# Optimization experiments

Measured on AMD Instinct MI355X. Metric: run time of the kernel, lower is better.

The kernel has to match this reference:

```python
import jax, jax.numpy as jnp
import numpy as np

D_MODEL, D_STATE, D_CONV, EXPAND = 1024, 16, 4, 2
D_INNER = EXPAND * D_MODEL
BATCH, SEQ = 2, 2048


def setup_inputs() -> dict:
    key = jax.random.key(0)
    ks = jax.random.split(key, 10)
    inv = lambda n: 1.0 / np.sqrt(n)
    return {
        "x": jax.random.normal(ks[0], (BATCH, SEQ, D_MODEL), jnp.float32),
        "in_proj_w": jax.random.uniform(ks[1], (2 * D_INNER, D_MODEL), jnp.float32, -inv(D_MODEL), inv(D_MODEL)),
        "conv_w": jax.random.uniform(ks[2], (D_INNER, D_INNER, D_CONV), jnp.float32, -inv(D_INNER * D_CONV), inv(D_INNER * D_CONV)),
        "conv_b": jax.random.uniform(ks[3], (D_INNER,), jnp.float32, -inv(D_INNER * D_CONV), inv(D_INNER * D_CONV)),
        "dt_w": jax.random.uniform(ks[4], (D_INNER, D_INNER), jnp.float32, -inv(D_INNER), inv(D_INNER)),
        "dt_b": jax.random.uniform(ks[5], (D_INNER,), jnp.float32, -inv(D_INNER), inv(D_INNER)),
        "A_log": jax.random.normal(ks[6], (D_INNER, D_STATE), jnp.float32) * 0.01,
        "D": jnp.ones((D_INNER,), jnp.float32),
        "B_w": jax.random.uniform(ks[7], (D_STATE, D_INNER), jnp.float32, -inv(D_INNER), inv(D_INNER)),
        "C_w": jax.random.uniform(ks[8], (D_STATE, D_INNER), jnp.float32, -inv(D_INNER), inv(D_INNER)),
        "out_w": jax.random.uniform(ks[9], (D_MODEL, D_INNER), jnp.float32, -inv(D_INNER), inv(D_INNER)),
    }


def _forward(x, in_proj_w, conv_w, conv_b, dt_w, dt_b, A_log, D, B_w, C_w, out_w):
    xz = x @ in_proj_w.T                      # [b, l, 2*d_inner]
    xc, z = jnp.split(xz, 2, axis=-1)
    # causal depthful conv1d (full channel mixing, left-padded)
    h = jnp.transpose(xc, (0, 2, 1))          # [b, d, l]
    h = jnp.pad(h, ((0, 0), (0, 0), (D_CONV - 1, 0)))
    h = jax.lax.conv_general_dilated(h, conv_w, (1,), 'VALID',
                                     dimension_numbers=('NCH', 'OIH', 'NCH'))
    h = h + conv_b[None, :, None]
    u = jnp.transpose(h, (0, 2, 1))           # [b, l, d_inner]

    dt = jnp.clip(jax.nn.sigmoid(u @ dt_w.T + dt_b), 1e-4, 1.0)  # [b, l, d]
    A = -jnp.exp(A_log)                       # [d, n]
    Bm = u @ B_w.T                            # [b, l, n]
    Cm = u @ C_w.T                            # [b, l, n]

    # time-major scan over the recurrence
    u_t = jnp.transpose(u, (1, 0, 2))
    dt_t = jnp.transpose(dt, (1, 0, 2))
    B_t = jnp.transpose(Bm, (1, 0, 2))
    C_t = jnp.transpose(Cm, (1, 0, 2))

    def step(state, inp):
        ut, dtt, bt, ct = inp                 # [b,d], [b,d], [b,n], [b,n]
        dA = jnp.exp(jnp.clip(dtt[:, :, None] * A, -5.0, 5.0))   # [b,d,n]
        dB = dtt[:, :, None] * bt[:, None, :] * ut[:, :, None]   # [b,d,n]
        state = dA * state + dB + 1e-6
        y = jnp.sum(state * ct[:, None, :], axis=-1) + D * ut    # [b,d]
        return state, y

    state0 = jnp.zeros((x.shape[0], D_INNER, D_STATE), x.dtype)
    _, ys = jax.lax.scan(step, state0, (u_t, dt_t, B_t, C_t))
    y = jnp.transpose(ys, (1, 0, 2))          # [b, l, d_inner]
    y = y * jax.nn.silu(z)
    return y @ out_w.T                        # [b, l, d_model]


def reference(x, in_proj_w, conv_w, conv_b, dt_w, dt_b, A_log, D, B_w, C_w, out_w):
    return _forward(x, in_proj_w, conv_w, conv_b, dt_w, dt_b, A_log, D, B_w, C_w, out_w)
```

## Files before the change

### kernel.cpp

```cpp
#include <hip/hip_runtime.h>

#define BATCHN 2
#define SEQL   2048
#define DM     1024
#define DI     2048
#define DSN    16
#define MTOT   (BATCHN * SEQL)
#define PADL   (SEQL + 3)
#define NC     64
#define CL     (SEQL / NC)
#define BCKS   8

typedef __attribute__((ext_vector_type(8))) __bf16 bf16x8;
typedef __attribute__((ext_vector_type(4))) float f32x4;

__device__ __forceinline__ unsigned short f2b(float f) {
    union { float f; unsigned u; } v; v.f = f;
    unsigned r = v.u + 0x7FFF + ((v.u >> 16) & 1);
    return (unsigned short)(r >> 16);
}
__device__ __forceinline__ float b2f(unsigned short b) {
    union { float f; unsigned u; } v; v.u = ((unsigned)b) << 16;
    return v.f;
}

__device__ __forceinline__ void gl_lds16(const void* g, void* l) {
    __builtin_amdgcn_global_load_lds(
        (const __attribute__((address_space(1))) unsigned int*)g,
        (__attribute__((address_space(3))) unsigned int*)l, 16, 0, 0);
}

__device__ __forceinline__ void swz(int& bx, int& by) {
    int gx = gridDim.x, gy = gridDim.y;
    int lin = blockIdx.y * gx + blockIdx.x;
    int xcd = lin & 7, k = lin >> 3;
    int rw = gx >> 1, rh = gy >> 2;
    by = (xcd >> 1) * rh + k / rw;
    bx = (xcd & 1) * rw + k % rw;
}

#define NB_CW4  (DI * DI / 4 / 256)
#define NB_TP   ((DM / 32) * (DI / 32))
#define NB_IPZ  (DI * DM / 4 / 256)
#define NB_DTW  (DI * DI / 4 / 256)
#define NB_OW   (DM * DI / 4 / 256)
#define NB_BW   (DSN * DI / 4 / 256 + 1)
#define NB_XCVT (MTOT * DM / 4 / 256)
#define NB_XZ   ((BATCHN * 3 * DM + 255) / 256)
#define NB_CVT_ALL (NB_CW4 + NB_TP + NB_IPZ + NB_DTW + NB_OW + 2 * NB_BW + NB_XCVT + NB_XZ)

__global__ void __launch_bounds__(256)
cvt_all(const float* __restrict__ x, const float* __restrict__ convw,
        const float* __restrict__ ipw, const float* __restrict__ dtw,
        const float* __restrict__ ow, const float* __restrict__ bw,
        const float* __restrict__ cw,
        unsigned short* __restrict__ xpad, unsigned short* __restrict__ wk,
        unsigned short* __restrict__ Pt, unsigned short* __restrict__ ipz,
        unsigned short* __restrict__ dtwb, unsigned short* __restrict__ owb,
        unsigned short* __restrict__ bcb)
{
    __shared__ float tile[32][33];
    int blk = blockIdx.x;
    int t = threadIdx.x;
    if (blk < NB_CW4) {
        int g = blk * 256 + t;
        int i = g * 4;
        const float4* cw4 = (const float4*)convw;
        float4 v0 = cw4[i + 0], v1 = cw4[i + 1], v2 = cw4[i + 2], v3 = cw4[i + 3];
#pragma unroll
        for (int k = 0; k < 4; ++k) {
            float e0 = (&v0.x)[k], e1 = (&v1.x)[k], e2 = (&v2.x)[k], e3 = (&v3.x)[k];
            ushort4 o;
            o.x = f2b(e0); o.y = f2b(e1); o.z = f2b(e2); o.w = f2b(e3);
            ((ushort4*)(wk + (size_t)k * DI * DI))[g] = o;
        }
        return;
    }
    blk -= NB_CW4;
    if (blk < NB_TP) {
        int ct = (blk & 31) * 32, it = (blk >> 5) * 32;
        int tx = t & 31, ty = t >> 5;
#pragma unroll
        for (int r = 0; r < 4; ++r)
            tile[ty + r * 8][tx] = ipw[(size_t)(it + ty + r * 8) * DM + ct + tx];
        __syncthreads();
#pragma unroll
        for (int r = 0; r < 4; ++r)
            Pt[(size_t)(ct + ty + r * 8) * DI + it + tx] = f2b(tile[tx][ty + r * 8]);
        return;
    }
    blk -= NB_TP;
    if (blk < NB_IPZ + NB_DTW + NB_OW + 2 * NB_BW) {
        const float* src;
        unsigned short* dst;
        int n4;
        if (blk < NB_IPZ) {
            src = ipw + (size_t)DI * DM; dst = ipz; n4 = DI * DM / 4;
        } else if ((blk -= NB_IPZ) < NB_DTW) {
            src = dtw; dst = dtwb; n4 = DI * DI / 4;
        } else if ((blk -= NB_DTW) < NB_OW) {
            src = ow; dst = owb; n4 = DM * DI / 4;
        } else if ((blk -= NB_OW) < NB_BW) {
            src = bw; dst = bcb; n4 = DSN * DI / 4;
        } else {
            blk -= NB_BW;
            src = cw; dst = bcb + (size_t)DSN * DI; n4 = DSN * DI / 4;
        }
        int i = blk * 256 + t;
        if (i < n4) {
            float4 v = ((const float4*)src)[i];
            ushort4 o;
            o.x = f2b(v.x); o.y = f2b(v.y); o.z = f2b(v.z); o.w = f2b(v.w);
            ((ushort4*)dst)[i] = o;
        }
        return;
    }
    blk -= NB_IPZ + NB_DTW + NB_OW + 2 * NB_BW;
    if (blk < NB_XCVT) {
        int i = blk * 256 + t;
        int b = i >> 19;
        float4 v = ((const float4*)x)[i];
        ushort4 o;
        o.x = f2b(v.x); o.y = f2b(v.y); o.z = f2b(v.z); o.w = f2b(v.w);
        ((ushort4*)xpad)[i + (b + 1) * (3 * DM / 4)] = o;
        return;
    }
    blk -= NB_XCVT;
    {
        int i = blk * 256 + t;
        if (i < BATCHN * 3 * DM) {
            int b = i / (3 * DM);
            int r = i % (3 * DM);
            xpad[(size_t)b * PADL * DM + r] = 0;
        }
    }
}

template<int MODE>
__global__ void __launch_bounds__(256)
gemm_bt(const unsigned short* __restrict__ Abase,
        const unsigned short* __restrict__ Bbase,
        const float* __restrict__ bias,
        unsigned short* __restrict__ out_bf,
        float* __restrict__ out_f,
        int K)
{
    __shared__ __align__(16) unsigned short As[128 * 64];
    __shared__ __align__(16) unsigned short Bs[128 * 64];

    const int t = threadIdx.x;
    const int lane = t & 63;
    const int wave = t >> 6;
    const int wm = wave & 1, wn = wave >> 1;
    int bx, by;
    swz(bx, by);
    const int m0 = by * 128, n0 = bx * 128;
    const int srow = t >> 3;
    const int scol = (t & 7) * 8;
    const int gcol = (((t & 7) ^ (srow & 7))) * 8;

    f32x4 acc[4][4];
#pragma unroll
    for (int i = 0; i < 4; ++i)
#pragma unroll
        for (int j = 0; j < 4; ++j)
            acc[i][j] = f32x4{0.f, 0.f, 0.f, 0.f};

    const unsigned short* arow[4];
    const unsigned short* brow[4];
#pragma unroll
    for (int i = 0; i < 4; ++i) {
        int rg = m0 + srow + i * 32;
        arow[i] = Abase + (size_t)rg * K;
        int ng = n0 + srow + i * 32;
        brow[i] = Bbase + (size_t)ng * K;
    }
    for (int k0 = 0; k0 < K; k0 += 64) {
#pragma unroll
        for (int i = 0; i < 4; ++i)
            gl_lds16(arow[i] + k0 + gcol, &As[(size_t)(srow + i * 32) * 64 + scol]);
#pragma unroll
        for (int i = 0; i < 4; ++i)
            gl_lds16(brow[i] + k0 + gcol, &Bs[(size_t)(srow + i * 32) * 64 + scol]);
        __syncthreads();
        const int qa = (lane >> 4) * 8;
        const int am = lane & 15;
        const int sw = (am & 7) << 3;
#pragma unroll
        for (int kk = 0; kk < 64; kk += 32) {
            bf16x8 af[4], bfv[4];
#pragma unroll
            for (int i = 0; i < 4; ++i)
                af[i] = *(const bf16x8*)&As[(wm * 64 + i * 16 + am) * 64 + ((kk + qa) ^ sw)];
#pragma unroll
            for (int j = 0; j < 4; ++j)
                bfv[j] = *(const bf16x8*)&Bs[(wn * 64 + j * 16 + am) * 64 + ((kk + qa) ^ sw)];
#pragma unroll
            for (int i = 0; i < 4; ++i)
#pragma unroll
                for (int j = 0; j < 4; ++j)
                    acc[i][j] = __builtin_amdgcn_mfma_f32_16x16x32_bf16(
                        af[i], bfv[j], acc[i][j], 0, 0, 0);
        }
        __syncthreads();
    }

    const int erow0 = m0 + wm * 64;
    const int ecol0 = n0 + wn * 64 + (lane & 15);
    const int rq = (lane >> 4) * 4;
#pragma unroll
    for (int i = 0; i < 4; ++i) {
#pragma unroll
        for (int j = 0; j < 4; ++j) {
            int col = ecol0 + j * 16;
#pragma unroll
            for (int r = 0; r < 4; ++r) {
                int row = erow0 + i * 16 + rq + r;
                float v = acc[i][j][r];
                if (MODE == 3) {
                    out_f[(size_t)row * DM + col] = v;
                } else {
                    out_bf[(size_t)row * DI + col] = f2b(v);
                }
            }
        }
    }
}

#define STAGE(buf, kt) do { \
    const int kc_ = ((kt) & NTM) << 6; \
    gl_lds16(pA + 0 * 64 * SA + kc_, &lds[(buf) * 16384 + ldsA + 0 * 4096]); \
    gl_lds16(pA + 1 * 64 * SA + kc_, &lds[(buf) * 16384 + ldsA + 1 * 4096]); \
    gl_lds16(pA + 2 * 64 * SA + kc_, &lds[(buf) * 16384 + ldsA + 2 * 4096]); \
    gl_lds16(pA + 3 * 64 * SA + kc_, &lds[(buf) * 16384 + ldsA + 3 * 4096]); \
    gl_lds16(pB + 0 * 64 * SB + kc_, &lds[32768 + (buf) * 8192 + ldsB + 0 * 4096]); \
    gl_lds16(pB + 1 * 64 * SB + kc_, &lds[32768 + (buf) * 8192 + ldsB + 1 * 4096]); \
} while (0)

#define LOADF(AF, BF, buf) do { \
    const unsigned short* _ab = &lds[(buf) * 16384 + arow]; \
    const unsigned short* _bb = &lds[32768 + (buf) * 8192 + brow]; \
    _Pragma("unroll") \
    for (int _i = 0; _i < 4; ++_i) { \
        AF[_i][0] = *(const bf16x8*)&_ab[_i * 1024 + c0]; \
        AF[_i][1] = *(const bf16x8*)&_ab[_i * 1024 + c1]; \
    } \
    _Pragma("unroll") \
    for (int _j = 0; _j < 4; ++_j) { \
        BF[_j][0] = *(const bf16x8*)&_bb[_j * 1024 + c0]; \
        BF[_j][1] = *(const bf16x8*)&_bb[_j * 1024 + c1]; \
    } \
} while (0)

#define MME(AF, BF) do { \
    _Pragma("unroll") \
    for (int _i = 0; _i < 4; ++_i) \
    _Pragma("unroll") \
    for (int _j = 0; _j < 4; ++_j) { \
        acc[_i][_j] = __builtin_amdgcn_mfma_f32_16x16x32_bf16(AF[_i][0], BF[_j][0], acc[_i][_j], 0, 0, 0); \
        acc[_i][_j] = __builtin_amdgcn_mfma_f32_16x16x32_bf16(AF[_i][1], BF[_j][1], acc[_i][_j], 0, 0, 0); \
    } \
} while (0)

template<int MODE>
__global__ void __launch_bounds__(512, 1)
gemm8(const unsigned short* __restrict__ Abase,
      const unsigned short* __restrict__ Bbase,
      const float* __restrict__ bias,
      unsigned short* __restrict__ out_bf,
      float* __restrict__ out_f)
{
    constexpr int K   = (MODE == 0) ? 1024 : (MODE == 1) ? 4096 : 2048;
    constexpr int SA  = (MODE == 2 || MODE == 4) ? 2048 : 1024;
    constexpr int SB  = (MODE == 0) ? 1024 : (MODE == 1) ? 4096 : 2048;
    constexpr int NT  = K / 64;
    constexpr int NTM = NT - 1;
    constexpr int NI  = NT / 2;
    (void)out_f;

    __shared__ __align__(16) unsigned short lds[49152];

    const int t = threadIdx.x;
    const int lane = t & 63;
    const int wave = t >> 6;
    const int wm = wave >> 1;
    const int wn = wave & 1;
    int bx, by;
    swz(bx, by);
    const int m0 = by * 256, n0 = bx * 128;

    const unsigned short* Ap;
    if (MODE == 0)      Ap = Abase + ((size_t)(m0 >> 11) * PADL + 3 + (m0 & 2047)) * DM;
    else if (MODE == 1) Ap = Abase + ((size_t)(m0 >> 11) * PADL + (m0 & 2047)) * DM;
    else if (MODE == 4) Ap = Abase + (size_t)blockIdx.z * DI * DI + (size_t)m0 * SA;
    else                Ap = Abase + (size_t)m0 * SA;
    const unsigned short* Bp = Bbase + (size_t)n0 * SB;

    const int strow = t >> 3;
    const int gcs = ((t & 7) ^ (strow & 7)) * 8;
    const unsigned short* pA = Ap + (size_t)strow * SA + gcs;
    const unsigned short* pB = Bp + (size_t)strow * SB + gcs;
    const int ldsA = t * 8;
    const int ldsB = t * 8;

    const int am = lane & 15;
    const int qa = (lane >> 4) << 3;
    const int sw = (am & 7) << 3;
    const int c0 = qa ^ sw;
    const int c1 = (32 + qa) ^ sw;
    const int arow = (wm * 64 + am) * 64;
    const int brow = (wn * 64 + am) * 64;

    f32x4 acc[4][4];
#pragma unroll
    for (int i = 0; i < 4; ++i)
#pragma unroll
        for (int j = 0; j < 4; ++j)
            acc[i][j] = f32x4{0.f, 0.f, 0.f, 0.f};

    bf16x8 aX[4][2], bX[4][2], aY[4][2], bY[4][2];

    STAGE(0, 0);
    STAGE(1, 1);
    asm volatile("s_waitcnt vmcnt(6)" ::: "memory");
    __builtin_amdgcn_s_barrier();
    __builtin_amdgcn_sched_barrier(0);
    LOADF(aX, bX, 0);

#pragma unroll 1
    for (int it = 0; it < NI; ++it) {
        asm volatile("s_waitcnt lgkmcnt(0)" ::: "memory");
        __builtin_amdgcn_s_barrier();
        __builtin_amdgcn_sched_barrier(0);
        STAGE(0, 2 * it + 2);
        asm volatile("s_waitcnt vmcnt(6)" ::: "memory");
        __builtin_amdgcn_s_barrier();
        __builtin_amdgcn_sched_barrier(0);
        LOADF(aY, bY, 1);
        __builtin_amdgcn_s_setprio(1);
        MME(aX, bX);
        __builtin_amdgcn_s_setprio(0);
        asm volatile("s_waitcnt lgkmcnt(0)" ::: "memory");
        __builtin_amdgcn_s_barrier();
        __builtin_amdgcn_sched_barrier(0);
        STAGE(1, 2 * it + 3);
        asm volatile("s_waitcnt vmcnt(6)" ::: "memory");
        __builtin_amdgcn_s_barrier();
        __builtin_amdgcn_sched_barrier(0);
        LOADF(aX, bX, 0);
        __builtin_amdgcn_s_setprio(1);
        MME(aY, bY);
        __builtin_amdgcn_s_setprio(0);
    }

    asm volatile("s_waitcnt vmcnt(0) lgkmcnt(0)" ::: "memory");

    const int rq = (lane >> 4) << 2;
    const int er = m0 + wm * 64;
    const int ec = n0 + wn * 64 + am;
#pragma unroll
    for (int mi = 0; mi < 4; ++mi) {
#pragma unroll
        for (int nj = 0; nj < 4; ++nj) {
            int col = ec + nj * 16;
#pragma unroll
            for (int r = 0; r < 4; ++r) {
                int row = er + mi * 16 + rq + r;
                float v = acc[mi][nj][r];
                if (MODE == 0) {
                    out_bf[(size_t)row * DI + col] = f2b(v);
                } else if (MODE == 1) {
                    v += bias[col];
                    out_bf[(size_t)row * DI + col] = f2b(v);
                } else if (MODE == 2) {
                    v += bias[col];
                    float s = 1.f / (1.f + __expf(-v));
                    s = fminf(fmaxf(s, 1e-4f), 1.f);
                    out_bf[(size_t)row * DI + col] = f2b(s);
                } else {
                    out_bf[(size_t)row * 4096 + (size_t)blockIdx.z * 1024 + col] = f2b(v);
                }
            }
        }
    }
}

__global__ void __launch_bounds__(256)
bc_mfma(const unsigned short* __restrict__ u,
        const unsigned short* __restrict__ w,
        float* __restrict__ pc)
{
    const int t = threadIdx.x;
    const int lane = t & 63;
    const int wave = t >> 6;
    const int ks = blockIdx.x;
    const int m0 = blockIdx.y * 128 + wave * 32;
    const int am = lane & 15, quad = lane >> 4;

    f32x4 acc[2][2];
#pragma unroll
    for (int i = 0; i < 2; ++i)
#pragma unroll
        for (int j = 0; j < 2; ++j)
            acc[i][j] = f32x4{0.f, 0.f, 0.f, 0.f};

    const int kbase = ks * (DI / BCKS);
    const unsigned short* ur0 = u + (size_t)(m0 + am) * DI;
    const unsigned short* ur1 = u + (size_t)(m0 + 16 + am) * DI;
    const unsigned short* wr0 = w + (size_t)am * DI;
    const unsigned short* wr1 = w + (size_t)(16 + am) * DI;
#pragma unroll 2
    for (int kk = 0; kk < DI / BCKS; kk += 32) {
        int k = kbase + kk + quad * 8;
        bf16x8 a0 = *(const bf16x8*)(ur0 + k);
        bf16x8 a1 = *(const bf16x8*)(ur1 + k);
        bf16x8 b0 = *(const bf16x8*)(wr0 + k);
        bf16x8 b1 = *(const bf16x8*)(wr1 + k);
        acc[0][0] = __builtin_amdgcn_mfma_f32_16x16x32_bf16(a0, b0, acc[0][0], 0, 0, 0);
        acc[0][1] = __builtin_amdgcn_mfma_f32_16x16x32_bf16(a0, b1, acc[0][1], 0, 0, 0);
        acc[1][0] = __builtin_amdgcn_mfma_f32_16x16x32_bf16(a1, b0, acc[1][0], 0, 0, 0);
        acc[1][1] = __builtin_amdgcn_mfma_f32_16x16x32_bf16(a1, b1, acc[1][1], 0, 0, 0);
    }
    float* base = pc + (size_t)ks * MTOT * 32;
#pragma unroll
    for (int i = 0; i < 2; ++i)
#pragma unroll
        for (int j = 0; j < 2; ++j)
#pragma unroll
            for (int r = 0; r < 4; ++r) {
                int row = m0 + i * 16 + quad * 4 + r;
                int col = j * 16 + am;
                base[(size_t)row * 32 + col] = acc[i][j][r];
            }
}

__global__ void __launch_bounds__(256)
scan_p1(const unsigned short* __restrict__ dt_bf,
        const unsigned short* __restrict__ u_bf,
        const float* __restrict__ pc,
        const float* __restrict__ A_log,
        float* __restrict__ Pbuf,
        float* __restrict__ Sb,
        float* __restrict__ bcf)
{
    const int t = threadIdx.x;
    const int blk = blockIdx.x;
    const int c  = blk & (NC - 1);
    const int dh = (blk >> 6) & 7;
    const int b  = blk >> 9;
    const int d  = dh * 256 + t;

    const size_t rowbase = (size_t)b * SEQL + (size_t)c * CL;

    __shared__ float sm[CL][32];
    for (int idx = t; idx < CL * 32; idx += 256) {
        int r = idx >> 5, n = idx & 31;
        size_t base = (rowbase + r) * 32 + n;
        float s = pc[base];
#pragma unroll
        for (int ks = 1; ks < BCKS; ++ks)
            s += pc[(size_t)ks * (MTOT * 32) + base];
        sm[r][n] = s;
        if (dh == 0) bcf[base] = s;
    }

    float Adn[16];
    {
        const float4* ar = (const float4*)(A_log + (size_t)d * DSN);
#pragma unroll
        for (int q = 0; q < 4; ++q) {
            float4 v = ar[q];
            Adn[q * 4 + 0] = -__expf(v.x);
            Adn[q * 4 + 1] = -__expf(v.y);
            Adn[q * 4 + 2] = -__expf(v.z);
            Adn[q * 4 + 3] = -__expf(v.w);
        }
    }
    float s[16], P[16];
#pragma unroll
    for (int n = 0; n < 16; ++n) { s[n] = 0.f; P[n] = 1.f; }

    __syncthreads();

    for (int l0 = 0; l0 < CL; l0 += 4) {
        float dt4[4], u4[4];
#pragma unroll
        for (int j = 0; j < 4; ++j) {
            size_t rb = rowbase + l0 + j;
            dt4[j] = b2f(dt_bf[rb * DI + d]);
            u4[j] = b2f(u_bf[rb * DI + d]);
        }
#pragma unroll
        for (int j = 0; j < 4; ++j) {
            const float4* Br = (const float4*)(&sm[l0 + j][0]);
            float Bn[16];
#pragma unroll
            for (int q = 0; q < 4; ++q) {
                float4 v = Br[q];
                Bn[q * 4 + 0] = v.x; Bn[q * 4 + 1] = v.y;
                Bn[q * 4 + 2] = v.z; Bn[q * 4 + 3] = v.w;
            }
            float dt = dt4[j];
            float dBu = dt * u4[j];
#pragma unroll
            for (int n = 0; n < 16; ++n) {
                float x = dt * Adn[n];
                x = fminf(fmaxf(x, -5.f), 5.f);
                float dA = __expf(x);
                P[n] *= dA;
                s[n] = dA * s[n] + (dBu * Bn[n] + 1e-6f);
            }
        }
    }
    size_t ob = (((size_t)c * BATCHN + b) * DI + d) * DSN;
#pragma unroll
    for (int q = 0; q < 4; ++q) {
        ((float4*)(Pbuf + ob))[q] = make_float4(P[q*4], P[q*4+1], P[q*4+2], P[q*4+3]);
        ((float4*)(Sb + ob))[q] = make_float4(s[q*4], s[q*4+1], s[q*4+2], s[q*4+3]);
    }
}

__global__ void __launch_bounds__(256)
scan_p2(const float* __restrict__ Pbuf,
        float* __restrict__ Sb)
{
    const int i = blockIdx.x * 256 + threadIdx.x;
    const int stride = BATCHN * DI * DSN;
    float s = 0.f;
    for (int c0 = 0; c0 < NC; c0 += 8) {
        float Pv[8], Sv[8];
#pragma unroll
        for (int j = 0; j < 8; ++j) {
            size_t idx = (size_t)(c0 + j) * stride + i;
            Pv[j] = Pbuf[idx];
            Sv[j] = Sb[idx];
        }
#pragma unroll
        for (int j = 0; j < 8; ++j) {
            size_t idx = (size_t)(c0 + j) * stride + i;
            Sb[idx] = s;
            s = Pv[j] * s + Sv[j];
        }
    }
}

__global__ void __launch_bounds__(256)
scan_p3(const unsigned short* __restrict__ dt_bf,
        const unsigned short* __restrict__ u_bf,
        const float* __restrict__ bcf,
        const unsigned short* __restrict__ z_bf,
        const float* __restrict__ A_log,
        const float* __restrict__ Dvec,
        const float* __restrict__ Ib,
        unsigned short* __restrict__ y_bf)
{
    const int t = threadIdx.x;
    const int blk = blockIdx.x;
    const int c  = blk & (NC - 1);
    const int dh = (blk >> 6) & 7;
    const int b  = blk >> 9;
    const int d  = dh * 256 + t;

    float Adn[16];
    {
        const float4* ar = (const float4*)(A_log + (size_t)d * DSN);
#pragma unroll
        for (int q = 0; q < 4; ++q) {
            float4 v = ar[q];
            Adn[q * 4 + 0] = -__expf(v.x);
            Adn[q * 4 + 1] = -__expf(v.y);
            Adn[q * 4 + 2] = -__expf(v.z);
            Adn[q * 4 + 3] = -__expf(v.w);
        }
    }
    const float Dd = Dvec[d];
    float s[16];
    {
        size_t ib = (((size_t)c * BATCHN + b) * DI + d) * DSN;
#pragma unroll
        for (int q = 0; q < 4; ++q) {
            float4 v = ((const float4*)(Ib + ib))[q];
            s[q * 4 + 0] = v.x; s[q * 4 + 1] = v.y;
            s[q * 4 + 2] = v.z; s[q * 4 + 3] = v.w;
        }
    }

    const size_t rowbase = (size_t)b * SEQL + (size_t)c * CL;
    for (int l0 = 0; l0 < CL; l0 += 4) {
        float dt4[4], u4[4], z4[4];
#pragma unroll
        for (int j = 0; j < 4; ++j) {
            size_t rb = rowbase + l0 + j;
            dt4[j] = b2f(dt_bf[rb * DI + d]);
            u4[j] = b2f(u_bf[rb * DI + d]);
            z4[j] = b2f(z_bf[rb * DI + d]);
        }
#pragma unroll
        for (int j = 0; j < 4; ++j) {
            size_t rb = rowbase + l0 + j;
            const float4* Br = (const float4*)(bcf + rb * 32);
            float Bn[16], Cn[16];
#pragma unroll
            for (int q = 0; q < 4; ++q) {
                float4 v = Br[q];
                Bn[q * 4 + 0] = v.x; Bn[q * 4 + 1] = v.y;
                Bn[q * 4 + 2] = v.z; Bn[q * 4 + 3] = v.w;
                float4 w = Br[q + 4];
                Cn[q * 4 + 0] = w.x; Cn[q * 4 + 1] = w.y;
                Cn[q * 4 + 2] = w.z; Cn[q * 4 + 3] = w.w;
            }
            float dt = dt4[j];
            float dBu = dt * u4[j];
            float y = 0.f;
#pragma unroll
            for (int n = 0; n < 16; ++n) {
                float x = dt * Adn[n];
                x = fminf(fmaxf(x, -5.f), 5.f);
                float dA = __expf(x);
                s[n] = dA * s[n] + (dBu * Bn[n] + 1e-6f);
                y += s[n] * Cn[n];
            }
            y += Dd * u4[j];
            float zz = z4[j];
            y *= zz / (1.f + __expf(-zz));
            y_bf[rb * DI + d] = f2b(y);
        }
    }
}

extern "C" void kernel_launch(void* const* d_in, const int* in_sizes, int n_in,
                              void* d_out, int out_size, void* d_ws, size_t ws_size,
                              hipStream_t stream) {
    const float* x     = (const float*)d_in[0];
    const float* ipw   = (const float*)d_in[1];
    const float* convw = (const float*)d_in[2];
    const float* convb = (const float*)d_in[3];
    const float* dtw   = (const float*)d_in[4];
    const float* dtb   = (const float*)d_in[5];
    const float* alog  = (const float*)d_in[6];
    const float* dvec  = (const float*)d_in[7];
    const float* bw    = (const float*)d_in[8];
    const float* cwm   = (const float*)d_in[9];
    const float* ow    = (const float*)d_in[10];
    float* out = (float*)d_out;

    char* ws = (char*)d_ws;
    unsigned short* wk_bf  = (unsigned short*)(ws);
    unsigned short* dt_bf  = (unsigned short*)(ws);
    float*          Pbuf   = (float*)(ws + 16777216);
    unsigned short* y_bf   = (unsigned short*)(ws + 16777216);
    unsigned short* mk_bf  = (unsigned short*)(ws + 33554432);
    float*          Sb     = (float*)(ws + 33554432);
    unsigned short* xpad   = (unsigned short*)(ws + 50331648);
    float*          pc_f   = (float*)(ws + 50331648);
    unsigned short* z_bf   = (unsigned short*)(ws + 58732544);
    unsigned short* Pt_bf  = (unsigned short*)(ws + 58732544);
    unsigned short* ipz_bf = (unsigned short*)(ws + 75509760);
    unsigned short* dtw_bf = (unsigned short*)(ws + 79704064);
    unsigned short* ow_bf  = (unsigned short*)(ws + 88092672);
    unsigned short* bc_bf  = (unsigned short*)(ws + 92286976);
    float*          bc_f   = (float*)(ws + 92418048);
    unsigned short* u_bf   = (unsigned short*)(ws + 92942336);

    cvt_all<<<NB_CVT_ALL, 256, 0, stream>>>(x, convw, ipw, dtw, ow, bw, cwm,
                                            xpad, wk_bf, Pt_bf, ipz_bf, dtw_bf,
                                            ow_bf, bc_bf);

    gemm8<4><<<dim3(8, 8, 4), 512, 0, stream>>>(wk_bf, Pt_bf, nullptr, mk_bf, nullptr);
    gemm8<0><<<dim3(16, 16), 512, 0, stream>>>(xpad, ipz_bf, nullptr, z_bf, nullptr);
    gemm8<1><<<dim3(16, 16), 512, 0, stream>>>(xpad, mk_bf, convb, u_bf, nullptr);
    bc_mfma<<<dim3(BCKS, MTOT / 128), 256, 0, stream>>>(u_bf, bc_bf, pc_f);
    gemm8<2><<<dim3(16, 16), 512, 0, stream>>>(u_bf, dtw_bf, dtb, dt_bf, nullptr);
    scan_p1<<<BATCHN * 8 * NC, 256, 0, stream>>>(dt_bf, u_bf, pc_f, alog, Pbuf, Sb, bc_f);
    scan_p2<<<BATCHN * DI * DSN / 256, 256, 0, stream>>>(Pbuf, Sb);
    scan_p3<<<BATCHN * 8 * NC, 256, 0, stream>>>(dt_bf, u_bf, bc_f, z_bf, alog, dvec, Sb, y_bf);
    gemm_bt<3><<<dim3(8, 32), 256, 0, stream>>>(y_bf, ow_bf, nullptr, nullptr, out, DI);
}
```

Measured before the change: 454.1 us.

## Split GEMM K dimension across two wave groups with LDS reduction

Restructures the gemm8 main loop so the 8 waves form two groups that each process half of the K range. Each wave now holds a 128x64 accumulator tile (8x4 MFMA tiles) and loads 32-wide K slices into separate LDS buffers. At the end the two groups' partial sums are combined through LDS before the epilogue. This raises the number of MFMAs per LDS fragment load and simplifies the pipeline, at the cost of doubled accumulator registers, an extra reduction pass with syncs, and shallower per-step K slices.

```diff
diff --git a/kernel.cpp b/kernel.cpp
--- a/kernel.cpp
+++ b/kernel.cpp
@@ -227,39 +227,14 @@
     }
 }
 
-#define STAGE(buf, kt) do { \
-    const int kc_ = ((kt) & NTM) << 6; \
-    gl_lds16(pA + 0 * 64 * SA + kc_, &lds[(buf) * 16384 + ldsA + 0 * 4096]); \
-    gl_lds16(pA + 1 * 64 * SA + kc_, &lds[(buf) * 16384 + ldsA + 1 * 4096]); \
-    gl_lds16(pA + 2 * 64 * SA + kc_, &lds[(buf) * 16384 + ldsA + 2 * 4096]); \
-    gl_lds16(pA + 3 * 64 * SA + kc_, &lds[(buf) * 16384 + ldsA + 3 * 4096]); \
-    gl_lds16(pB + 0 * 64 * SB + kc_, &lds[32768 + (buf) * 8192 + ldsB + 0 * 4096]); \
-    gl_lds16(pB + 1 * 64 * SB + kc_, &lds[32768 + (buf) * 8192 + ldsB + 1 * 4096]); \
-} while (0)
-
-#define LOADF(AF, BF, buf) do { \
-    const unsigned short* _ab = &lds[(buf) * 16384 + arow]; \
-    const unsigned short* _bb = &lds[32768 + (buf) * 8192 + brow]; \
-    _Pragma("unroll") \
-    for (int _i = 0; _i < 4; ++_i) { \
-        AF[_i][0] = *(const bf16x8*)&_ab[_i * 1024 + c0]; \
-        AF[_i][1] = *(const bf16x8*)&_ab[_i * 1024 + c1]; \
-    } \
-    _Pragma("unroll") \
-    for (int _j = 0; _j < 4; ++_j) { \
-        BF[_j][0] = *(const bf16x8*)&_bb[_j * 1024 + c0]; \
-        BF[_j][1] = *(const bf16x8*)&_bb[_j * 1024 + c1]; \
-    } \
-} while (0)
-
-#define MME(AF, BF) do { \
-    _Pragma("unroll") \
-    for (int _i = 0; _i < 4; ++_i) \
-    _Pragma("unroll") \
-    for (int _j = 0; _j < 4; ++_j) { \
-        acc[_i][_j] = __builtin_amdgcn_mfma_f32_16x16x32_bf16(AF[_i][0], BF[_j][0], acc[_i][_j], 0, 0, 0); \
-        acc[_i][_j] = __builtin_amdgcn_mfma_f32_16x16x32_bf16(AF[_i][1], BF[_j][1], acc[_i][_j], 0, 0, 0); \
-    } \
+
+#define STG2(buf, kt) do { const int kc_ = ((kt) & NTM) * 32; \
+    gl_lds16(pA0[0] + kc_, &lds[(buf) * 8192 + l8]); \
+    gl_lds16(pA1[0] + kc_, &lds[(buf) * 8192 + 4096 + l8]); \
+    gl_lds16(pB2[0] + kc_, &lds[32768 + (buf) * 4096 + l8]); \
+    gl_lds16(pA0[1] + kc_, &lds[16384 + (buf) * 8192 + l8]); \
+    gl_lds16(pA1[1] + kc_, &lds[16384 + (buf) * 8192 + 4096 + l8]); \
+    gl_lds16(pB2[1] + kc_, &lds[40960 + (buf) * 4096 + l8]); \
 } while (0)
 
 template<int MODE>
@@ -273,9 +248,9 @@
     constexpr int K   = (MODE == 0) ? 1024 : (MODE == 1) ? 4096 : 2048;
     constexpr int SA  = (MODE == 2 || MODE == 4) ? 2048 : 1024;
     constexpr int SB  = (MODE == 0) ? 1024 : (MODE == 1) ? 4096 : 2048;
-    constexpr int NT  = K / 64;
+    constexpr int KG  = K / 2;
+    constexpr int NT  = KG / 32;
     constexpr int NTM = NT - 1;
-    constexpr int NI  = NT / 2;
     (void)out_f;
 
     __shared__ __align__(16) unsigned short lds[49152];
@@ -283,8 +258,9 @@
     const int t = threadIdx.x;
     const int lane = t & 63;
     const int wave = t >> 6;
-    const int wm = wave >> 1;
-    const int wn = wave & 1;
+    const int g   = wave >> 2;
+    const int wm2 = (wave >> 1) & 1;
+    const int wn2 = wave & 1;
     int bx, by;
     swz(bx, by);
     const int m0 = by * 256, n0 = bx * 128;
@@ -296,89 +272,108 @@
     else                Ap = Abase + (size_t)m0 * SA;
     const unsigned short* Bp = Bbase + (size_t)n0 * SB;
 
-    const int strow = t >> 3;
-    const int gcs = ((t & 7) ^ (strow & 7)) * 8;
-    const unsigned short* pA = Ap + (size_t)strow * SA + gcs;
-    const unsigned short* pB = Bp + (size_t)strow * SB + gcs;
-    const int ldsA = t * 8;
-    const int ldsB = t * 8;
+    const int rA0 = t >> 2;
+    const int rA1 = (512 + t) >> 2;
+    const int qA  = t & 3;
+    const unsigned short* pA0[2];
+    const unsigned short* pA1[2];
+    const unsigned short* pB2[2];
+#pragma unroll
+    for (int gg = 0; gg < 2; ++gg) {
+        pA0[gg] = Ap + (size_t)rA0 * SA + (qA ^ (rA0 & 3)) * 8 + gg * KG;
+        pA1[gg] = Ap + (size_t)rA1 * SA + (qA ^ (rA1 & 3)) * 8 + gg * KG;
+        pB2[gg] = Bp + (size_t)rA0 * SB + (qA ^ (rA0 & 3)) * 8 + gg * KG;
+    }
+    const int l8 = t * 8;
 
     const int am = lane & 15;
-    const int qa = (lane >> 4) << 3;
-    const int sw = (am & 7) << 3;
-    const int c0 = qa ^ sw;
-    const int c1 = (32 + qa) ^ sw;
-    const int arow = (wm * 64 + am) * 64;
-    const int brow = (wn * 64 + am) * 64;
-
-    f32x4 acc[4][4];
-#pragma unroll
-    for (int i = 0; i < 4; ++i)
+    const int quad = lane >> 4;
+    const int fsw = (quad ^ (am & 3)) * 8;
+    const int abase0 = g * 16384;
+    const int bbase0 = 32768 + g * 8192;
+    const int arow0 = (wm2 * 128 + am) * 32;
+    const int brow0 = (wn2 * 64 + am) * 32;
+
+    f32x4 acc[8][4];
+#pragma unroll
+    for (int i = 0; i < 8; ++i)
 #pragma unroll
         for (int j = 0; j < 4; ++j)
             acc[i][j] = f32x4{0.f, 0.f, 0.f, 0.f};
 
-    bf16x8 aX[4][2], bX[4][2], aY[4][2], bY[4][2];
-
-    STAGE(0, 0);
-    STAGE(1, 1);
-    asm volatile("s_waitcnt vmcnt(6)" ::: "memory");
-    __builtin_amdgcn_s_barrier();
-    __builtin_amdgcn_sched_barrier(0);
-    LOADF(aX, bX, 0);
-
+    STG2(0, 0);
 #pragma unroll 1
-    for (int it = 0; it < NI; ++it) {
-        asm volatile("s_waitcnt lgkmcnt(0)" ::: "memory");
-        __builtin_amdgcn_s_barrier();
-        __builtin_amdgcn_sched_barrier(0);
-        STAGE(0, 2 * it + 2);
+    for (int kt = 0; kt < NT; ++kt) {
+        const int buf = kt & 1;
+        STG2(buf ^ 1, kt + 1);
         asm volatile("s_waitcnt vmcnt(6)" ::: "memory");
         __builtin_amdgcn_s_barrier();
         __builtin_amdgcn_sched_barrier(0);
-        LOADF(aY, bY, 1);
+        bf16x8 a[8], b[4];
+#pragma unroll
+        for (int mi = 0; mi < 8; ++mi)
+            a[mi] = *(const bf16x8*)&lds[abase0 + buf * 8192 + arow0 + mi * 512 + fsw];
+#pragma unroll
+        for (int nj = 0; nj < 4; ++nj)
+            b[nj] = *(const bf16x8*)&lds[bbase0 + buf * 4096 + brow0 + nj * 512 + fsw];
+        asm volatile("s_waitcnt lgkmcnt(0)" ::: "memory");
+        __builtin_amdgcn_sched_barrier(0);
         __builtin_amdgcn_s_setprio(1);
-        MME(aX, bX);
+#pragma unroll
+        for (int mi = 0; mi < 8; ++mi)
+#pragma unroll
+            for (int nj = 0; nj < 4; ++nj)
+                acc[mi][nj] = __builtin_amdgcn_mfma_f32_16x16x32_bf16(
+                    a[mi], b[nj], acc[mi][nj], 0, 0, 0);
         __builtin_amdgcn_s_setprio(0);
-        asm volatile("s_waitcnt lgkmcnt(0)" ::: "memory");
         __builtin_amdgcn_s_barrier();
         __builtin_amdgcn_sched_barrier(0);
-        STAGE(1, 2 * it + 3);
-        asm volatile("s_waitcnt vmcnt(6)" ::: "memory");
-        __builtin_amdgcn_s_barrier();
-        __builtin_amdgcn_sched_barrier(0);
-        LOADF(aX, bX, 0);
-        __builtin_amdgcn_s_setprio(1);
-        MME(aY, bY);
-        __builtin_amdgcn_s_setprio(0);
-    }
-
-    asm volatile("s_waitcnt vmcnt(0) lgkmcnt(0)" ::: "memory");
-
-    const int rq = (lane >> 4) << 2;
-    const int er = m0 + wm * 64;
-    const int ec = n0 + wn * 64 + am;
-#pragma unroll
-    for (int mi = 0; mi < 4; ++mi) {
-#pragma unroll
-        for (int nj = 0; nj < 4; ++nj) {
-            int col = ec + nj * 16;
-#pragma unroll
-            for (int r = 0; r < 4; ++r) {
-                int row = er + mi * 16 + rq + r;
-                float v = acc[mi][nj][r];
-                if (MODE == 0) {
-                    out_bf[(size_t)row * DI + col] = f2b(v);
-                } else if (MODE == 1) {
-                    v += bias[col];
-                    out_bf[(size_t)row * DI + col] = f2b(v);
-                } else if (MODE == 2) {
-                    v += bias[col];
-                    float s = 1.f / (1.f + __expf(-v));
-                    s = fminf(fmaxf(s, 1e-4f), 1.f);
-                    out_bf[(size_t)row * DI + col] = f2b(s);
-                } else {
-                    out_bf[(size_t)row * 4096 + (size_t)blockIdx.z * 1024 + col] = f2b(v);
+    }
+    asm volatile("s_waitcnt vmcnt(0)" ::: "memory");
+
+    float* red = (float*)lds;
+    constexpr int RS = 64 * 132;
+    const int rq = quad * 4;
+#pragma unroll 1
+    for (int round = 0; round < 2; ++round) {
+        __syncthreads();
+        if (g == 1 && wm2 == round) {
+            float* slot = red + wn2 * RS;
+#pragma unroll
+            for (int mi = 0; mi < 8; ++mi)
+#pragma unroll
+                for (int nj = 0; nj < 4; ++nj)
+                    *(f32x4*)&slot[(nj * 16 + am) * 132 + mi * 16 + rq] = acc[mi][nj];
+        }
+        __syncthreads();
+        if (g == 0 && wm2 == round) {
+            const float* slot = red + wn2 * RS;
+            const int er = m0 + wm2 * 128;
+            const int ec = n0 + wn2 * 64 + am;
+#pragma unroll
+            for (int mi = 0; mi < 8; ++mi) {
+#pragma unroll
+                for (int nj = 0; nj < 4; ++nj) {
+                    f32x4 o = *(const f32x4*)&slot[(nj * 16 + am) * 132 + mi * 16 + rq];
+                    int col = ec + nj * 16;
+#pragma unroll
+                    for (int r = 0; r < 4; ++r) {
+                        int row = er + mi * 16 + rq + r;
+                        float v = acc[mi][nj][r] + o[r];
+                        if (MODE == 0) {
+                            out_bf[(size_t)row * DI + col] = f2b(v);
+                        } else if (MODE == 1) {
+                            v += bias[col];
+                            out_bf[(size_t)row * DI + col] = f2b(v);
+                        } else if (MODE == 2) {
+                            v += bias[col];
+                            float s = 1.f / (1.f + __expf(-v));
+                            s = fminf(fmaxf(s, 1e-4f), 1.f);
+                            out_bf[(size_t)row * DI + col] = f2b(s);
+                        } else {
+                            out_bf[(size_t)row * 4096 + (size_t)blockIdx.z * 1024 + col] = f2b(v);
+                        }
+                    }
                 }
             }
         }
```

Measured after the change: 508.0 us. 11.9% more time.
